# Performance work log

Measured on AMD Instinct MI355X. Metric: run time of the kernel, lower is better.

## Reference

```python
import jax, jax.numpy as jnp
import numpy as np

VOCAB, V_DIM, TOPICS, K_DIM = 50000, 256, 512, 256


def setup_inputs() -> dict:
    key = jax.random.key(0)
    k1, k2, k3, k4, k5 = jax.random.split(key, 5)
    bw = np.sqrt(3.0 / V_DIM)
    bt = np.sqrt(3.0 / K_DIM)
    return {
        "w2v": jax.random.uniform(k1, (VOCAB, V_DIM), jnp.float32, -bw, bw),
        "t2v": jax.random.uniform(k2, (TOPICS, K_DIM), jnp.float32, -bt, bt),
        "A": jax.random.normal(k3, (V_DIM, K_DIM), jnp.float32),
        "B": jax.random.normal(k4, (V_DIM, K_DIM), jnp.float32),
        "sigma": jax.random.uniform(k5, (1,), jnp.float32),  # torch.rand(1) lifted to input
    }


def reference(w2v, t2v, A, B, sigma):
    # s[:, i] = (w2v[i] @ B) @ t2v.T  -> batched: [T, V]
    s = jnp.einsum('tk,vk->tv', t2v, w2v @ B)  # [topic_size, vocab_size]
    # softmax over topic dim (dim=0 in original)
    alpha = jax.nn.softmax(s, axis=0)  # [T, V]
    # mu[:, i] = A @ sum_t alpha[t,i] * t2v[t]
    ctx = jnp.einsum('tk,tv->kv', t2v, alpha)  # [k_dim, V]
    mu = A @ ctx  # [v_dim, V]
    diff = w2v.T - mu  # [v_dim, V]
    P = (1.0 / sigma[0]) * jnp.sum(diff * diff, axis=0, keepdims=True)  # [1, V]
    RL = jnp.sum((alpha - jnp.mean(alpha, axis=1, keepdims=True)) ** 2)
    return alpha, P, RL, s, sigma
```

## Files before the change

kernel.cpp:

```cpp
#include <hip/hip_runtime.h>

#define VOCAB 50000
#define VDIM 256
#define TOPICS 512
#define VT 32
#define NBLK 1563
#define NXCD 8

#define SYNC_LDS() asm volatile("s_waitcnt lgkmcnt(0)\n\ts_barrier" ::: "memory")

typedef unsigned int uint;
typedef unsigned short ushort;
using short8 = __attribute__((ext_vector_type(8))) short;
using f32x4  = __attribute__((ext_vector_type(4))) float;

__device__ __forceinline__ ushort bf16_rne(float f) {
  uint u = __float_as_uint(f);
  u += 0x7FFFu + ((u >> 16) & 1u);
  return (ushort)(u >> 16);
}
__device__ __forceinline__ float bf16f(ushort h) {
  return __uint_as_float(((uint)h) << 16);
}
__device__ __forceinline__ uint packbf2(float a, float b) {
  return (uint)bf16_rne(a) | ((uint)bf16_rne(b) << 16);
}

__device__ __forceinline__ int xcd_swizzle(int orig, int nwg) {
  const int q = nwg / NXCD, r = nwg % NXCD;
  const int xcd = orig % NXCD, i = orig / NXCD;
  return (xcd < r ? xcd * (q + 1) : r * (q + 1) + (xcd - r) * q) + i;
}

__global__ __launch_bounds__(512) void precompute(
    const float* __restrict__ t2v, const float* __restrict__ A,
    const float* __restrict__ B,
    ushort* __restrict__ tBp, ushort* __restrict__ Atp)
{
  __shared__ float row[256];
  const int b = blockIdx.x, tid = threadIdx.x;
  if (b < TOPICS) {
    const int t = b;
    if (tid < 256) row[tid] = t2v[(size_t)t * 256 + tid];
    __syncthreads();
    if (tid < 256) {
      const int d = tid;
      const float4* rv = (const float4*)row;
      const float4* bv = (const float4*)(B + (size_t)d * 256);
      float acc = 0.f;
#pragma unroll 8
      for (int k = 0; k < 64; ++k) {
        float4 r = rv[k], x = bv[k];
        acc += r.x * x.x + r.y * x.y + r.z * x.z + r.w * x.w;
      }
      const int tile = t >> 4, ks = d >> 5;
      const int lane = (t & 15) | (((d >> 3) & 3) << 4);
      const int e = d & 7;
      tBp[((size_t)tile * 8 + ks) * 512 + lane * 8 + e] = bf16_rne(acc);
    }
  } else {
    const int d = b - TOPICS;
    if (tid < 256) row[tid] = A[(size_t)d * 256 + tid];
    __syncthreads();
    const int t = tid;
    const float4* rv = (const float4*)row;
    const float4* tv = (const float4*)(t2v + (size_t)t * 256);
    float acc = 0.f;
#pragma unroll 8
    for (int k = 0; k < 64; ++k) {
      float4 r = rv[k], x = tv[k];
      acc += r.x * x.x + r.y * x.y + r.z * x.z + r.w * x.w;
    }
    const int dtile = d >> 4, ks = t >> 5;
    const int lane = (d & 15) | (((t >> 3) & 3) << 4);
    const int e = t & 7;
    Atp[((size_t)dtile * 16 + ks) * 512 + lane * 8 + e] = bf16_rne(acc);
  }
}

__global__ __launch_bounds__(256, 4) void fused_main(
    const float* __restrict__ w2v,
    const ushort* __restrict__ tBp, const ushort* __restrict__ Atp,
    const float* __restrict__ sigma,
    float* __restrict__ out_alpha, float* __restrict__ out_P,
    float* __restrict__ out_s,
    float* __restrict__ part_rs, float* __restrict__ part_ss, int do_rl)
{
  __shared__ __align__(16) char smem[33792];
  ushort (*Whi)[264] = (ushort (*)[264])smem;
  ushort (*Wlo)[264] = (ushort (*)[264])(smem + 16896);
  ushort (*PA)[520]  = (ushort (*)[520])smem;
  float  (*SST)[32]  = (float  (*)[32])smem;
  __shared__ float red[4][VT];
  __shared__ float rs_lds[TOPICS];

  const int tid  = threadIdx.x;
  const int wave = tid >> 6, lane = tid & 63;
  const int lr = lane & 15, lg = lane >> 4;
  const int bid = xcd_swizzle(blockIdx.x, NBLK);
  const int vb = bid * VT;

  const ushort* sbase = tBp + (size_t)wave * 32768 + lane * 8;
  short8 Ah[4];
#pragma unroll
  for (int i = 0; i < 4; ++i)
    Ah[i] = *(const short8*)(sbase + (size_t)i * 4096);

#pragma unroll
  for (int it = 0; it < 8; ++it) {
    int j = tid + (it << 8);
    int v = j >> 6, q = j & 63;
    int vr = min(vb + v, VOCAB - 1);
    float4 x = *(const float4*)(w2v + (size_t)vr * 256 + (q << 2));
    float xs[4] = {x.x, x.y, x.z, x.w};
    ushort h[4], l[4];
#pragma unroll
    for (int i = 0; i < 4; ++i) {
      ushort hi = bf16_rne(xs[i]);
      h[i] = hi;
      l[i] = bf16_rne(xs[i] - bf16f(hi));
    }
    *(uint2*)&Whi[v][q << 2] = make_uint2((uint)h[0] | ((uint)h[1] << 16),
                                          (uint)h[2] | ((uint)h[3] << 16));
    *(uint2*)&Wlo[v][q << 2] = make_uint2((uint)l[0] | ((uint)l[1] << 16),
                                          (uint)l[2] | ((uint)l[3] << 16));
  }
  SYNC_LDS();

  f32x4 acc[8][2];
#pragma unroll
  for (int mi = 0; mi < 8; ++mi)
#pragma unroll
    for (int nj = 0; nj < 2; ++nj) acc[mi][nj] = (f32x4){0.f, 0.f, 0.f, 0.f};

#pragma unroll
  for (int ks = 0; ks < 8; ++ks) {
    const int k0 = (ks << 5) + (lg << 3);
    short8 bh[2], bl[2];
#pragma unroll
    for (int nj = 0; nj < 2; ++nj) {
      bh[nj] = *(const short8*)&Whi[(nj << 4) + lr][k0];
      bl[nj] = *(const short8*)&Wlo[(nj << 4) + lr][k0];
    }
#pragma unroll
    for (int mi = 0; mi < 8; ++mi) {
      const int n = (ks << 3) + mi;
      short8 ah = Ah[n & 3];
      if (n + 4 < 64) {
        const int n4 = n + 4;
        Ah[n & 3] = *(const short8*)(sbase + (size_t)(n4 & 7) * 4096
                                           + (size_t)(n4 >> 3) * 512);
      }
#pragma unroll
      for (int nj = 0; nj < 2; ++nj) {
        acc[mi][nj] = __builtin_amdgcn_mfma_f32_16x16x32_bf16(ah, bh[nj], acc[mi][nj], 0, 0, 0);
        acc[mi][nj] = __builtin_amdgcn_mfma_f32_16x16x32_bf16(ah, bl[nj], acc[mi][nj], 0, 0, 0);
      }
    }
  }
  SYNC_LDS();

#pragma unroll
  for (int ph = 0; ph < 2; ++ph) {
    if ((wave >> 1) == ph) {
#pragma unroll
      for (int mi = 0; mi < 8; ++mi) {
        const int tb = ((wave & 1) << 7) + (mi << 4) + (lg << 2);
#pragma unroll
        for (int r = 0; r < 4; ++r) {
          const int t = tb + r, sw = (t & 7) << 2;
#pragma unroll
          for (int nj = 0; nj < 2; ++nj)
            SST[t][((nj << 4) + lr) ^ sw] = acc[mi][nj][r];
        }
      }
    }
    SYNC_LDS();
    {
      const int row = tid >> 3, cb = (tid & 7) << 2;
      const int v = vb + cb;
#pragma unroll
      for (int it = 0; it < 8; ++it) {
        const int t = row + (it << 5);
        if (v < VOCAB)
          *(float4*)(out_s + (size_t)(t + (ph << 8)) * VOCAB + v) =
              *(const float4*)&SST[t][cb ^ ((t & 7) << 2)];
      }
    }
    SYNC_LDS();
  }

  float gmax[2];
  {
    float pm[2] = {-3.4e38f, -3.4e38f};
#pragma unroll
    for (int mi = 0; mi < 8; ++mi)
#pragma unroll
      for (int nj = 0; nj < 2; ++nj)
#pragma unroll
        for (int r = 0; r < 4; ++r) pm[nj] = fmaxf(pm[nj], acc[mi][nj][r]);
#pragma unroll
    for (int nj = 0; nj < 2; ++nj) {
      pm[nj] = fmaxf(pm[nj], __shfl_xor(pm[nj], 16));
      pm[nj] = fmaxf(pm[nj], __shfl_xor(pm[nj], 32));
    }
    if (lg == 0) { red[wave][lr] = pm[0]; red[wave][16 + lr] = pm[1]; }
  }
  SYNC_LDS();
#pragma unroll
  for (int nj = 0; nj < 2; ++nj) {
    const int c = (nj << 4) + lr;
    gmax[nj] = fmaxf(fmaxf(red[0][c], red[1][c]), fmaxf(red[2][c], red[3][c]));
  }
  SYNC_LDS();

  const ushort* mbase = Atp + (size_t)wave * 32768 + lane * 8;
  short8 Mh[4];
#pragma unroll
  for (int i = 0; i < 4; ++i)
    Mh[i] = *(const short8*)(mbase + (size_t)i * 8192);

  float inv[2];
  {
    float ps[2] = {0.f, 0.f};
#pragma unroll
    for (int mi = 0; mi < 8; ++mi)
#pragma unroll
      for (int nj = 0; nj < 2; ++nj)
#pragma unroll
        for (int r = 0; r < 4; ++r) {
          float e = __expf(acc[mi][nj][r] - gmax[nj]);
          acc[mi][nj][r] = e;
          ps[nj] += e;
        }
#pragma unroll
    for (int nj = 0; nj < 2; ++nj) {
      ps[nj] += __shfl_xor(ps[nj], 16);
      ps[nj] += __shfl_xor(ps[nj], 32);
    }
    if (lg == 0) { red[wave][lr] = ps[0]; red[wave][16 + lr] = ps[1]; }
  }
  SYNC_LDS();
#pragma unroll
  for (int nj = 0; nj < 2; ++nj) {
    const int c = (nj << 4) + lr;
    inv[nj] = 1.0f / (red[0][c] + red[1][c] + red[2][c] + red[3][c]);
  }
  SYNC_LDS();

#pragma unroll
  for (int mi = 0; mi < 8; ++mi)
#pragma unroll
    for (int nj = 0; nj < 2; ++nj)
#pragma unroll
      for (int r = 0; r < 4; ++r) acc[mi][nj][r] *= inv[nj];

#pragma unroll
  for (int ph = 0; ph < 2; ++ph) {
    if ((wave >> 1) == ph) {
#pragma unroll
      for (int mi = 0; mi < 8; ++mi) {
        const int tb = ((wave & 1) << 7) + (mi << 4) + (lg << 2);
#pragma unroll
        for (int r = 0; r < 4; ++r) {
          const int t = tb + r, sw = (t & 7) << 2;
#pragma unroll
          for (int nj = 0; nj < 2; ++nj)
            SST[t][((nj << 4) + lr) ^ sw] = acc[mi][nj][r];
        }
      }
    }
    SYNC_LDS();
    {
      const int row = tid >> 3, cb = (tid & 7) << 2;
      const int v = vb + cb;
#pragma unroll
      for (int it = 0; it < 8; ++it) {
        const int t = row + (it << 5);
        if (v < VOCAB)
          *(float4*)(out_alpha + (size_t)(t + (ph << 8)) * VOCAB + v) =
              *(const float4*)&SST[t][cb ^ ((t & 7) << 2)];
      }
    }
    SYNC_LDS();
  }

  float ssq = 0.f;
#pragma unroll
  for (int mi = 0; mi < 8; ++mi) {
    const int tb = (wave << 7) + (mi << 4) + (lg << 2);
#pragma unroll
    for (int nj = 0; nj < 2; ++nj) {
      uint2 pw;
      pw.x = packbf2(acc[mi][nj][0], acc[mi][nj][1]);
      pw.y = packbf2(acc[mi][nj][2], acc[mi][nj][3]);
      *(uint2*)&PA[(nj << 4) + lr][tb] = pw;
    }
    if (do_rl) {
#pragma unroll
      for (int r = 0; r < 4; ++r) {
        float rowp = 0.f;
#pragma unroll
        for (int nj = 0; nj < 2; ++nj) {
          float a = acc[mi][nj][r];
          float am = (vb + (nj << 4) + lr < VOCAB) ? a : 0.f;
          rowp += am;
          ssq = fmaf(am, am, ssq);
        }
        rowp += __shfl_xor(rowp, 1);
        rowp += __shfl_xor(rowp, 2);
        rowp += __shfl_xor(rowp, 4);
        rowp += __shfl_xor(rowp, 8);
        if (lr == 0) rs_lds[tb + r] = rowp;
      }
    }
  }
  SYNC_LDS();

  f32x4 macc[4][2];
#pragma unroll
  for (int mi = 0; mi < 4; ++mi)
#pragma unroll
    for (int nj = 0; nj < 2; ++nj) macc[mi][nj] = (f32x4){0.f, 0.f, 0.f, 0.f};

#pragma unroll
  for (int ks = 0; ks < 16; ++ks) {
    const int k0 = (ks << 5) + (lg << 3);
    short8 pb[2];
#pragma unroll
    for (int nj = 0; nj < 2; ++nj)
      pb[nj] = *(const short8*)&PA[(nj << 4) + lr][k0];
#pragma unroll
    for (int mi = 0; mi < 4; ++mi) {
      const int n = (ks << 2) + mi;
      short8 ah = Mh[n & 3];
      if (n + 4 < 64) {
        const int n4 = n + 4;
        Mh[n & 3] = *(const short8*)(mbase + (size_t)(n4 & 3) * 8192
                                           + (size_t)(n4 >> 2) * 512);
      }
#pragma unroll
      for (int nj = 0; nj < 2; ++nj)
        macc[mi][nj] = __builtin_amdgcn_mfma_f32_16x16x32_bf16(ah, pb[nj], macc[mi][nj], 0, 0, 0);
    }
  }

  {
    float pp[2] = {0.f, 0.f};
#pragma unroll
    for (int mi = 0; mi < 4; ++mi) {
      const int dbase = (wave << 6) + (mi << 4) + (lg << 2);
#pragma unroll
      for (int nj = 0; nj < 2; ++nj) {
        const int vr = min(vb + (nj << 4) + lr, VOCAB - 1);
        float4 w = *(const float4*)(w2v + (size_t)vr * 256 + dbase);
        float d0 = w.x - macc[mi][nj][0];
        float d1 = w.y - macc[mi][nj][1];
        float d2 = w.z - macc[mi][nj][2];
        float d3 = w.w - macc[mi][nj][3];
        pp[nj] += d0 * d0 + d1 * d1 + d2 * d2 + d3 * d3;
      }
    }
#pragma unroll
    for (int nj = 0; nj < 2; ++nj) {
      pp[nj] += __shfl_xor(pp[nj], 16);
      pp[nj] += __shfl_xor(pp[nj], 32);
    }
    if (lg == 0) { red[wave][lr] = pp[0]; red[wave][16 + lr] = pp[1]; }
  }
  SYNC_LDS();
  if (tid < VT) {
    float sum = red[0][tid] + red[1][tid] + red[2][tid] + red[3][tid];
    const int v = vb + tid;
    if (v < VOCAB) out_P[v] = sum / sigma[0];
  }

  if (do_rl) {
    part_rs[(size_t)bid * TOPICS + tid]       = rs_lds[tid];
    part_rs[(size_t)bid * TOPICS + 256 + tid] = rs_lds[256 + tid];
    ssq += __shfl_xor(ssq, 1);
    ssq += __shfl_xor(ssq, 2);
    ssq += __shfl_xor(ssq, 4);
    ssq += __shfl_xor(ssq, 8);
    ssq += __shfl_xor(ssq, 16);
    ssq += __shfl_xor(ssq, 32);
    if (lane == 0) part_ss[bid * 4 + wave] = ssq;
  }
}

__global__ __launch_bounds__(256) void rl_pass2(
    const float* __restrict__ part_rs, float* __restrict__ rowsum)
{
  const int t = blockIdx.x;
  float s = 0.f;
  for (int i = threadIdx.x; i < NBLK; i += 256)
    s += part_rs[(size_t)i * TOPICS + t];
  __shared__ float lsum[4];
  const int lane = threadIdx.x & 63, wave = threadIdx.x >> 6;
#pragma unroll
  for (int off = 32; off > 0; off >>= 1) s += __shfl_xor(s, off);
  if (lane == 0) lsum[wave] = s;
  __syncthreads();
  if (threadIdx.x == 0) rowsum[t] = lsum[0] + lsum[1] + lsum[2] + lsum[3];
}

__global__ __launch_bounds__(512) void rl_final_new(
    const float* __restrict__ rowsum, const float* __restrict__ part_ss,
    const float* __restrict__ sigma, float* __restrict__ out_RL,
    float* __restrict__ out_sigma)
{
  const int t = threadIdx.x;
  float b = rowsum[t] * rowsum[t];
  float a = 0.f;
  for (int i = t; i < NBLK * 4; i += 512) a += part_ss[i];
  __shared__ float la[8], lb[8];
  const int lane = t & 63, wave = t >> 6;
#pragma unroll
  for (int off = 32; off > 0; off >>= 1) {
    a += __shfl_xor(a, off);
    b += __shfl_xor(b, off);
  }
  if (lane == 0) { la[wave] = a; lb[wave] = b; }
  __syncthreads();
  if (t == 0) {
    float sa = 0.f, sb = 0.f;
#pragma unroll
    for (int w = 0; w < 8; ++w) { sa += la[w]; sb += lb[w]; }
    out_RL[0] = sa - sb / (float)VOCAB;
    out_sigma[0] = sigma[0];
  }
}

__global__ __launch_bounds__(256) void row_reduce(
    const float* __restrict__ alpha, float* __restrict__ rowsum, float* __restrict__ ssum)
{
  const int t = blockIdx.x;
  const float4* base = (const float4*)(alpha + (size_t)t * VOCAB);
  float rs = 0.f, ss = 0.f;
  for (int i = threadIdx.x; i < VOCAB / 4; i += 256) {
    float4 a = base[i];
    rs += a.x + a.y + a.z + a.w;
    ss += a.x * a.x + a.y * a.y + a.z * a.z + a.w * a.w;
  }
  __shared__ float lr[4], ls[4];
  const int lane = threadIdx.x & 63, wave = threadIdx.x >> 6;
#pragma unroll
  for (int off = 32; off > 0; off >>= 1) {
    rs += __shfl_xor(rs, off);
    ss += __shfl_xor(ss, off);
  }
  if (lane == 0) { lr[wave] = rs; ls[wave] = ss; }
  __syncthreads();
  if (threadIdx.x == 0) {
    rowsum[t] = lr[0] + lr[1] + lr[2] + lr[3];
    ssum[t]   = ls[0] + ls[1] + ls[2] + ls[3];
  }
}

__global__ __launch_bounds__(512) void rl_final_old(
    const float* __restrict__ rowsum, const float* __restrict__ ssum,
    const float* __restrict__ sigma, float* __restrict__ out_RL,
    float* __restrict__ out_sigma)
{
  const int t = threadIdx.x;
  float a = ssum[t];
  float b = rowsum[t] * rowsum[t];
  __shared__ float la[8], lb[8];
  const int lane = t & 63, wave = t >> 6;
#pragma unroll
  for (int off = 32; off > 0; off >>= 1) {
    a += __shfl_xor(a, off);
    b += __shfl_xor(b, off);
  }
  if (lane == 0) { la[wave] = a; lb[wave] = b; }
  __syncthreads();
  if (t == 0) {
    float sa = 0.f, sb = 0.f;
#pragma unroll
    for (int w = 0; w < 8; ++w) { sa += la[w]; sb += lb[w]; }
    out_RL[0] = sa - sb / (float)VOCAB;
    out_sigma[0] = sigma[0];
  }
}

extern "C" void kernel_launch(void* const* d_in, const int* in_sizes, int n_in,
                              void* d_out, int out_size, void* d_ws, size_t ws_size,
                              hipStream_t stream) {
  const float* w2v   = (const float*)d_in[0];
  const float* t2v   = (const float*)d_in[1];
  const float* A     = (const float*)d_in[2];
  const float* B     = (const float*)d_in[3];
  const float* sigma = (const float*)d_in[4];

  float* out       = (float*)d_out;
  float* out_alpha = out;
  float* out_P     = out + (size_t)TOPICS * VOCAB;
  float* out_RL    = out_P + VOCAB;
  float* out_s     = out_RL + 1;
  float* out_sigma = out_s + (size_t)TOPICS * VOCAB;

  ushort* tBp = (ushort*)d_ws;
  ushort* Atp = tBp + (size_t)131072;
  float* tail = (float*)(Atp + (size_t)131072);
  float* part_rs = tail;
  float* part_ss = part_rs + (size_t)NBLK * TOPICS;
  float* rowsum  = part_ss + (size_t)NBLK * 4;
  size_t need = (size_t)(2 * 131072) * 2 +
                ((size_t)NBLK * TOPICS + (size_t)NBLK * 4 + TOPICS) * 4;
  const int do_rl = (ws_size >= need) ? 1 : 0;

  precompute<<<TOPICS + VDIM, 512, 0, stream>>>(t2v, A, B, tBp, Atp);

  fused_main<<<NBLK, 256, 0, stream>>>(w2v, tBp, Atp, sigma,
                                       out_alpha, out_P, out_s,
                                       part_rs, part_ss, do_rl);

  if (do_rl) {
    rl_pass2<<<TOPICS, 256, 0, stream>>>(part_rs, rowsum);
    rl_final_new<<<1, 512, 0, stream>>>(rowsum, part_ss, sigma, out_RL, out_sigma);
  } else {
    float* rs_old = tail;
    float* ss_old = rs_old + TOPICS;
    row_reduce<<<TOPICS, 256, 0, stream>>>(out_alpha, rs_old, ss_old);
    rl_final_old<<<1, 512, 0, stream>>>(rs_old, ss_old, sigma, out_RL, out_sigma);
  }
}
```

Baseline: 153.9 us.

## Double vocab tile per block to 64 with 512 threads and 8 waves

Widens each block's vocabulary tile from 32 to 64 columns and doubles the block to 512 threads (8 waves). Each wave now owns fewer topic rows but more vocab columns, so the bf16 topic/A operands streamed from global memory are reused across twice as many columns and the block count halves. The LDS staging tile grows to about 66 KB, and the XOR swizzle is replaced with a padded row stride of 66 floats. The larger LDS footprint and 512-thread blocks may cut occupancy, and the unswizzled transpose may cause bank conflicts.

```diff
diff --git a/kernel.cpp b/kernel.cpp
--- a/kernel.cpp
+++ b/kernel.cpp
@@ -3,8 +3,8 @@
 #define VOCAB 50000
 #define VDIM 256
 #define TOPICS 512
-#define VT 32
-#define NBLK 1563
+#define VT 64
+#define NBLK 782
 #define NXCD 8
 
 #define SYNC_LDS() asm volatile("s_waitcnt lgkmcnt(0)\n\ts_barrier" ::: "memory")
@@ -78,7 +78,7 @@
   }
 }
 
-__global__ __launch_bounds__(256, 4) void fused_main(
+__global__ __launch_bounds__(512, 4) void fused_main(
     const float* __restrict__ w2v,
     const ushort* __restrict__ tBp, const ushort* __restrict__ Atp,
     const float* __restrict__ sigma,
@@ -86,12 +86,12 @@
     float* __restrict__ out_s,
     float* __restrict__ part_rs, float* __restrict__ part_ss, int do_rl)
 {
-  __shared__ __align__(16) char smem[33792];
+  __shared__ __align__(16) char smem[67584];
   ushort (*Whi)[264] = (ushort (*)[264])smem;
-  ushort (*Wlo)[264] = (ushort (*)[264])(smem + 16896);
+  ushort (*Wlo)[264] = (ushort (*)[264])(smem + 33792);
   ushort (*PA)[520]  = (ushort (*)[520])smem;
-  float  (*SST)[32]  = (float  (*)[32])smem;
-  __shared__ float red[4][VT];
+  float  (*SST)[66]  = (float  (*)[66])smem;
+  __shared__ float red[8][VT];
   __shared__ float rs_lds[TOPICS];
 
   const int tid  = threadIdx.x;
@@ -100,7 +100,7 @@
   const int bid = xcd_swizzle(blockIdx.x, NBLK);
   const int vb = bid * VT;
 
-  const ushort* sbase = tBp + (size_t)wave * 32768 + lane * 8;
+  const ushort* sbase = tBp + (size_t)wave * 16384 + lane * 8;
   short8 Ah[4];
 #pragma unroll
   for (int i = 0; i < 4; ++i)
@@ -108,7 +108,7 @@
 
 #pragma unroll
   for (int it = 0; it < 8; ++it) {
-    int j = tid + (it << 8);
+    int j = tid + (it << 9);
     int v = j >> 6, q = j & 63;
     int vr = min(vb + v, VOCAB - 1);
     float4 x = *(const float4*)(w2v + (size_t)vr * 256 + (q << 2));
@@ -127,32 +127,29 @@
   }
   SYNC_LDS();
 
-  f32x4 acc[8][2];
-#pragma unroll
-  for (int mi = 0; mi < 8; ++mi)
-#pragma unroll
-    for (int nj = 0; nj < 2; ++nj) acc[mi][nj] = (f32x4){0.f, 0.f, 0.f, 0.f};
+  f32x4 acc[4][4];
+#pragma unroll
+  for (int mi = 0; mi < 4; ++mi)
+#pragma unroll
+    for (int nj = 0; nj < 4; ++nj) acc[mi][nj] = (f32x4){0.f, 0.f, 0.f, 0.f};
 
 #pragma unroll
   for (int ks = 0; ks < 8; ++ks) {
     const int k0 = (ks << 5) + (lg << 3);
-    short8 bh[2], bl[2];
-#pragma unroll
-    for (int nj = 0; nj < 2; ++nj) {
+    short8 bh[4], bl[4];
+#pragma unroll
+    for (int nj = 0; nj < 4; ++nj) {
       bh[nj] = *(const short8*)&Whi[(nj << 4) + lr][k0];
       bl[nj] = *(const short8*)&Wlo[(nj << 4) + lr][k0];
     }
 #pragma unroll
-    for (int mi = 0; mi < 8; ++mi) {
-      const int n = (ks << 3) + mi;
-      short8 ah = Ah[n & 3];
-      if (n + 4 < 64) {
-        const int n4 = n + 4;
-        Ah[n & 3] = *(const short8*)(sbase + (size_t)(n4 & 7) * 4096
-                                           + (size_t)(n4 >> 3) * 512);
-      }
-#pragma unroll
-      for (int nj = 0; nj < 2; ++nj) {
+    for (int mi = 0; mi < 4; ++mi) {
+      short8 ah = Ah[mi];
+      if (ks < 7)
+        Ah[mi] = *(const short8*)(sbase + (size_t)mi * 4096
+                                        + (size_t)(ks + 1) * 512);
+#pragma unroll
+      for (int nj = 0; nj < 4; ++nj) {
         acc[mi][nj] = __builtin_amdgcn_mfma_f32_16x16x32_bf16(ah, bh[nj], acc[mi][nj], 0, 0, 0);
         acc[mi][nj] = __builtin_amdgcn_mfma_f32_16x16x32_bf16(ah, bl[nj], acc[mi][nj], 0, 0, 0);
       }
@@ -162,71 +159,74 @@
 
 #pragma unroll
   for (int ph = 0; ph < 2; ++ph) {
-    if ((wave >> 1) == ph) {
-#pragma unroll
-      for (int mi = 0; mi < 8; ++mi) {
-        const int tb = ((wave & 1) << 7) + (mi << 4) + (lg << 2);
+    if ((wave >> 2) == ph) {
+#pragma unroll
+      for (int mi = 0; mi < 4; ++mi) {
+        const int tb = ((wave & 3) << 6) + (mi << 4) + (lg << 2);
 #pragma unroll
         for (int r = 0; r < 4; ++r) {
-          const int t = tb + r, sw = (t & 7) << 2;
-#pragma unroll
-          for (int nj = 0; nj < 2; ++nj)
-            SST[t][((nj << 4) + lr) ^ sw] = acc[mi][nj][r];
+          const int t = tb + r;
+#pragma unroll
+          for (int nj = 0; nj < 4; ++nj)
+            SST[t][(nj << 4) + lr] = acc[mi][nj][r];
         }
       }
     }
     SYNC_LDS();
     {
-      const int row = tid >> 3, cb = (tid & 7) << 2;
+      const int row = tid >> 4, cb = (tid & 15) << 2;
       const int v = vb + cb;
 #pragma unroll
       for (int it = 0; it < 8; ++it) {
         const int t = row + (it << 5);
         if (v < VOCAB)
           *(float4*)(out_s + (size_t)(t + (ph << 8)) * VOCAB + v) =
-              *(const float4*)&SST[t][cb ^ ((t & 7) << 2)];
+              *(const float4*)&SST[t][cb];
       }
     }
     SYNC_LDS();
   }
 
-  float gmax[2];
+  float gmax[4];
   {
-    float pm[2] = {-3.4e38f, -3.4e38f};
-#pragma unroll
-    for (int mi = 0; mi < 8; ++mi)
-#pragma unroll
-      for (int nj = 0; nj < 2; ++nj)
+    float pm[4] = {-3.4e38f, -3.4e38f, -3.4e38f, -3.4e38f};
+#pragma unroll
+    for (int mi = 0; mi < 4; ++mi)
+#pragma unroll
+      for (int nj = 0; nj < 4; ++nj)
 #pragma unroll
         for (int r = 0; r < 4; ++r) pm[nj] = fmaxf(pm[nj], acc[mi][nj][r]);
 #pragma unroll
-    for (int nj = 0; nj < 2; ++nj) {
+    for (int nj = 0; nj < 4; ++nj) {
       pm[nj] = fmaxf(pm[nj], __shfl_xor(pm[nj], 16));
       pm[nj] = fmaxf(pm[nj], __shfl_xor(pm[nj], 32));
-    }
-    if (lg == 0) { red[wave][lr] = pm[0]; red[wave][16 + lr] = pm[1]; }
-  }
-  SYNC_LDS();
-#pragma unroll
-  for (int nj = 0; nj < 2; ++nj) {
+      if (lg == 0) red[wave][(nj << 4) + lr] = pm[nj];
+    }
+  }
+  SYNC_LDS();
+#pragma unroll
+  for (int nj = 0; nj < 4; ++nj) {
     const int c = (nj << 4) + lr;
-    gmax[nj] = fmaxf(fmaxf(red[0][c], red[1][c]), fmaxf(red[2][c], red[3][c]));
-  }
-  SYNC_LDS();
-
-  const ushort* mbase = Atp + (size_t)wave * 32768 + lane * 8;
+    float m0 = fmaxf(fmaxf(red[0][c], red[1][c]), fmaxf(red[2][c], red[3][c]));
+    float m1 = fmaxf(fmaxf(red[4][c], red[5][c]), fmaxf(red[6][c], red[7][c]));
+    gmax[nj] = fmaxf(m0, m1);
+  }
+  SYNC_LDS();
+
+  const ushort* mbase = Atp + (size_t)wave * 16384 + lane * 8;
   short8 Mh[4];
-#pragma unroll
-  for (int i = 0; i < 4; ++i)
-    Mh[i] = *(const short8*)(mbase + (size_t)i * 8192);
-
-  float inv[2];
+  Mh[0] = *(const short8*)(mbase);
+  Mh[1] = *(const short8*)(mbase + 8192);
+  Mh[2] = *(const short8*)(mbase + 512);
+  Mh[3] = *(const short8*)(mbase + 8192 + 512);
+
+  float inv[4];
   {
-    float ps[2] = {0.f, 0.f};
-#pragma unroll
-    for (int mi = 0; mi < 8; ++mi)
-#pragma unroll
-      for (int nj = 0; nj < 2; ++nj)
+    float ps[4] = {0.f, 0.f, 0.f, 0.f};
+#pragma unroll
+    for (int mi = 0; mi < 4; ++mi)
+#pragma unroll
+      for (int nj = 0; nj < 4; ++nj)
 #pragma unroll
         for (int r = 0; r < 4; ++r) {
           float e = __expf(acc[mi][nj][r] - gmax[nj]);
@@ -234,52 +234,54 @@
           ps[nj] += e;
         }
 #pragma unroll
-    for (int nj = 0; nj < 2; ++nj) {
+    for (int nj = 0; nj < 4; ++nj) {
       ps[nj] += __shfl_xor(ps[nj], 16);
       ps[nj] += __shfl_xor(ps[nj], 32);
-    }
-    if (lg == 0) { red[wave][lr] = ps[0]; red[wave][16 + lr] = ps[1]; }
-  }
-  SYNC_LDS();
-#pragma unroll
-  for (int nj = 0; nj < 2; ++nj) {
+      if (lg == 0) red[wave][(nj << 4) + lr] = ps[nj];
+    }
+  }
+  SYNC_LDS();
+#pragma unroll
+  for (int nj = 0; nj < 4; ++nj) {
     const int c = (nj << 4) + lr;
-    inv[nj] = 1.0f / (red[0][c] + red[1][c] + red[2][c] + red[3][c]);
-  }
-  SYNC_LDS();
-
-#pragma unroll
-  for (int mi = 0; mi < 8; ++mi)
-#pragma unroll
-    for (int nj = 0; nj < 2; ++nj)
+    float s0 = (red[0][c] + red[1][c]) + (red[2][c] + red[3][c]);
+    float s1 = (red[4][c] + red[5][c]) + (red[6][c] + red[7][c]);
+    inv[nj] = 1.0f / (s0 + s1);
+  }
+  SYNC_LDS();
+
+#pragma unroll
+  for (int mi = 0; mi < 4; ++mi)
+#pragma unroll
+    for (int nj = 0; nj < 4; ++nj)
 #pragma unroll
       for (int r = 0; r < 4; ++r) acc[mi][nj][r] *= inv[nj];
 
 #pragma unroll
   for (int ph = 0; ph < 2; ++ph) {
-    if ((wave >> 1) == ph) {
-#pragma unroll
-      for (int mi = 0; mi < 8; ++mi) {
-        const int tb = ((wave & 1) << 7) + (mi << 4) + (lg << 2);
+    if ((wave >> 2) == ph) {
+#pragma unroll
+      for (int mi = 0; mi < 4; ++mi) {
+        const int tb = ((wave & 3) << 6) + (mi << 4) + (lg << 2);
 #pragma unroll
         for (int r = 0; r < 4; ++r) {
-          const int t = tb + r, sw = (t & 7) << 2;
-#pragma unroll
-          for (int nj = 0; nj < 2; ++nj)
-            SST[t][((nj << 4) + lr) ^ sw] = acc[mi][nj][r];
+          const int t = tb + r;
+#pragma unroll
+          for (int nj = 0; nj < 4; ++nj)
+            SST[t][(nj << 4) + lr] = acc[mi][nj][r];
         }
       }
     }
     SYNC_LDS();
     {
-      const int row = tid >> 3, cb = (tid & 7) << 2;
+      const int row = tid >> 4, cb = (tid & 15) << 2;
       const int v = vb + cb;
 #pragma unroll
       for (int it = 0; it < 8; ++it) {
         const int t = row + (it << 5);
         if (v < VOCAB)
           *(float4*)(out_alpha + (size_t)(t + (ph << 8)) * VOCAB + v) =
-              *(const float4*)&SST[t][cb ^ ((t & 7) << 2)];
+              *(const float4*)&SST[t][cb];
       }
     }
     SYNC_LDS();
@@ -287,10 +289,10 @@
 
   float ssq = 0.f;
 #pragma unroll
-  for (int mi = 0; mi < 8; ++mi) {
-    const int tb = (wave << 7) + (mi << 4) + (lg << 2);
-#pragma unroll
-    for (int nj = 0; nj < 2; ++nj) {
+  for (int mi = 0; mi < 4; ++mi) {
+    const int tb = (wave << 6) + (mi << 4) + (lg << 2);
+#pragma unroll
+    for (int nj = 0; nj < 4; ++nj) {
       uint2 pw;
       pw.x = packbf2(acc[mi][nj][0], acc[mi][nj][1]);
       pw.y = packbf2(acc[mi][nj][2], acc[mi][nj][3]);
@@ -301,7 +303,7 @@
       for (int r = 0; r < 4; ++r) {
         float rowp = 0.f;
 #pragma unroll
-        for (int nj = 0; nj < 2; ++nj) {
+        for (int nj = 0; nj < 4; ++nj) {
           float a = acc[mi][nj][r];
           float am = (vb + (nj << 4) + lr < VOCAB) ? a : 0.f;
           rowp += am;
@@ -317,41 +319,39 @@
   }
   SYNC_LDS();
 
-  f32x4 macc[4][2];
-#pragma unroll
-  for (int mi = 0; mi < 4; ++mi)
-#pragma unroll
-    for (int nj = 0; nj < 2; ++nj) macc[mi][nj] = (f32x4){0.f, 0.f, 0.f, 0.f};
+  f32x4 macc[2][4];
+#pragma unroll
+  for (int mi = 0; mi < 2; ++mi)
+#pragma unroll
+    for (int nj = 0; nj < 4; ++nj) macc[mi][nj] = (f32x4){0.f, 0.f, 0.f, 0.f};
 
 #pragma unroll
   for (int ks = 0; ks < 16; ++ks) {
     const int k0 = (ks << 5) + (lg << 3);
-    short8 pb[2];
-#pragma unroll
-    for (int nj = 0; nj < 2; ++nj)
+    short8 pb[4];
+#pragma unroll
+    for (int nj = 0; nj < 4; ++nj)
       pb[nj] = *(const short8*)&PA[(nj << 4) + lr][k0];
 #pragma unroll
-    for (int mi = 0; mi < 4; ++mi) {
-      const int n = (ks << 2) + mi;
+    for (int mi = 0; mi < 2; ++mi) {
+      const int n = (ks << 1) + mi;
       short8 ah = Mh[n & 3];
-      if (n + 4 < 64) {
-        const int n4 = n + 4;
-        Mh[n & 3] = *(const short8*)(mbase + (size_t)(n4 & 3) * 8192
-                                           + (size_t)(n4 >> 2) * 512);
-      }
-#pragma unroll
-      for (int nj = 0; nj < 2; ++nj)
+      if (n + 4 < 32)
+        Mh[n & 3] = *(const short8*)(mbase + (size_t)mi * 8192
+                                           + (size_t)(ks + 2) * 512);
+#pragma unroll
+      for (int nj = 0; nj < 4; ++nj)
         macc[mi][nj] = __builtin_amdgcn_mfma_f32_16x16x32_bf16(ah, pb[nj], macc[mi][nj], 0, 0, 0);
     }
   }
 
   {
-    float pp[2] = {0.f, 0.f};
-#pragma unroll
-    for (int mi = 0; mi < 4; ++mi) {
-      const int dbase = (wave << 6) + (mi << 4) + (lg << 2);
-#pragma unroll
-      for (int nj = 0; nj < 2; ++nj) {
+    float pp[4] = {0.f, 0.f, 0.f, 0.f};
+#pragma unroll
+    for (int mi = 0; mi < 2; ++mi) {
+      const int dbase = ((wave << 1) + mi) * 16 + (lg << 2);
+#pragma unroll
+      for (int nj = 0; nj < 4; ++nj) {
         const int vr = min(vb + (nj << 4) + lr, VOCAB - 1);
         float4 w = *(const float4*)(w2v + (size_t)vr * 256 + dbase);
         float d0 = w.x - macc[mi][nj][0];
@@ -362,29 +362,29 @@
       }
     }
 #pragma unroll
-    for (int nj = 0; nj < 2; ++nj) {
+    for (int nj = 0; nj < 4; ++nj) {
       pp[nj] += __shfl_xor(pp[nj], 16);
       pp[nj] += __shfl_xor(pp[nj], 32);
-    }
-    if (lg == 0) { red[wave][lr] = pp[0]; red[wave][16 + lr] = pp[1]; }
+      if (lg == 0) red[wave][(nj << 4) + lr] = pp[nj];
+    }
   }
   SYNC_LDS();
   if (tid < VT) {
-    float sum = red[0][tid] + red[1][tid] + red[2][tid] + red[3][tid];
+    float s0 = (red[0][tid] + red[1][tid]) + (red[2][tid] + red[3][tid]);
+    float s1 = (red[4][tid] + red[5][tid]) + (red[6][tid] + red[7][tid]);
     const int v = vb + tid;
-    if (v < VOCAB) out_P[v] = sum / sigma[0];
+    if (v < VOCAB) out_P[v] = (s0 + s1) / sigma[0];
   }
 
   if (do_rl) {
-    part_rs[(size_t)bid * TOPICS + tid]       = rs_lds[tid];
-    part_rs[(size_t)bid * TOPICS + 256 + tid] = rs_lds[256 + tid];
+    part_rs[(size_t)bid * TOPICS + tid] = rs_lds[tid];
     ssq += __shfl_xor(ssq, 1);
     ssq += __shfl_xor(ssq, 2);
     ssq += __shfl_xor(ssq, 4);
     ssq += __shfl_xor(ssq, 8);
     ssq += __shfl_xor(ssq, 16);
     ssq += __shfl_xor(ssq, 32);
-    if (lane == 0) part_ss[bid * 4 + wave] = ssq;
+    if (lane == 0) part_ss[bid * 8 + wave] = ssq;
   }
 }
 
@@ -412,7 +412,7 @@
   const int t = threadIdx.x;
   float b = rowsum[t] * rowsum[t];
   float a = 0.f;
-  for (int i = t; i < NBLK * 4; i += 512) a += part_ss[i];
+  for (int i = t; i < NBLK * 8; i += 512) a += part_ss[i];
   __shared__ float la[8], lb[8];
   const int lane = t & 63, wave = t >> 6;
 #pragma unroll
@@ -504,14 +504,14 @@
   float* tail = (float*)(Atp + (size_t)131072);
   float* part_rs = tail;
   float* part_ss = part_rs + (size_t)NBLK * TOPICS;
-  float* rowsum  = part_ss + (size_t)NBLK * 4;
+  float* rowsum  = part_ss + (size_t)NBLK * 8;
   size_t need = (size_t)(2 * 131072) * 2 +
-                ((size_t)NBLK * TOPICS + (size_t)NBLK * 4 + TOPICS) * 4;
+                ((size_t)NBLK * TOPICS + (size_t)NBLK * 8 + TOPICS) * 4;
   const int do_rl = (ws_size >= need) ? 1 : 0;
 
   precompute<<<TOPICS + VDIM, 512, 0, stream>>>(t2v, A, B, tBp, Atp);
 
-  fused_main<<<NBLK, 256, 0, stream>>>(w2v, tBp, Atp, sigma,
+  fused_main<<<NBLK, 512, 0, stream>>>(w2v, tBp, Atp, sigma,
                                        out_alpha, out_P, out_s,
                                        part_rs, part_ss, do_rl);
 
```

Measured after the change: 142.2 us, median of 2. 7.6% less time.
